# Performance work log

Hardware: AMD Instinct MI355X
Metric: run time of the kernel (lower is better)

## Reference

```python
import jax, jax.numpy as jnp
import numpy as np

N_HEADS = 16
N_KV_HEADS = 8
N_REP = 2
HEAD_DIM = 128
SOFTCAP = 50.0
NEG_INF = -2.3819763e38
ROPE_BASE = 10000.0


def _rotate_half(x):
    x1, x2 = jnp.split(x, 2, axis=-1)
    return jnp.concatenate((-x2, x1), axis=-1)


def _rope_cos_sin(seq_len, dtype):
    # Gemma2RotaryEmbedding: inv_freq over even dims, emb = cat(freqs, freqs)
    inv_freq = 1.0 / (ROPE_BASE ** (jnp.arange(0, HEAD_DIM, 2, dtype=jnp.float32) / HEAD_DIM))
    freqs = jnp.arange(seq_len, dtype=jnp.float32)[:, None] * inv_freq[None, :]  # [s, hd/2]
    emb = jnp.concatenate((freqs, freqs), axis=-1)  # [s, hd]
    return jnp.cos(emb).astype(dtype), jnp.sin(emb).astype(dtype)


def setup_inputs() -> dict:
    key = jax.random.key(0)
    ks = jax.random.split(key, 5)
    b, s, d = 2, 2048, 2048
    w_scale = 0.02
    return {
        "x": jax.random.normal(ks[0], (b, s, d), dtype=jnp.float32),
        "wq": jax.random.normal(ks[1], (N_HEADS * HEAD_DIM, d), dtype=jnp.float32) * w_scale,
        "wk": jax.random.normal(ks[2], (N_KV_HEADS * HEAD_DIM, d), dtype=jnp.float32) * w_scale,
        "wv": jax.random.normal(ks[3], (N_KV_HEADS * HEAD_DIM, d), dtype=jnp.float32) * w_scale,
        "wo": jax.random.normal(ks[4], (d, N_HEADS * HEAD_DIM), dtype=jnp.float32) * w_scale,
    }


def reference(x, wq, wk, wv, wo):
    b, s, d = x.shape
    # QKV projections (linear_fn = plain x @ W.T)
    xq = (x @ wq.T).reshape(b, s, N_HEADS, HEAD_DIM).transpose(0, 2, 1, 3)      # [b,h,s,hd]
    xk = (x @ wk.T).reshape(b, s, N_KV_HEADS, HEAD_DIM).transpose(0, 2, 1, 3)   # [b,kv,s,hd]
    xv = (x @ wv.T).reshape(b, s, N_KV_HEADS, HEAD_DIM).transpose(0, 2, 1, 3)
    # Gemma2 rotary on q, k
    cos, sin = _rope_cos_sin(s, x.dtype)  # [s,hd] each, broadcast over b,h
    xq = xq * cos + _rotate_half(xq) * sin
    xk = xk * cos + _rotate_half(xk) * sin
    # repeat_kv: expand kv heads to n_heads
    keys = jnp.repeat(xk, N_REP, axis=1)
    values = jnp.repeat(xv, N_REP, axis=1)
    # scores with scaling and Gemma2 logit softcapping
    scale = float(HEAD_DIM) ** -0.5
    scores = jnp.einsum("bhsd,bhtd->bhst", xq * scale, keys)
    scores = jnp.tanh(scores / SOFTCAP) * SOFTCAP
    # causal additive mask [s, t]
    q_pos = jnp.arange(s)[:, None]
    k_pos = jnp.arange(s)[None, :]
    mask = jnp.where(k_pos <= q_pos, 0.0, NEG_INF).astype(jnp.float32)
    scores = scores + mask  # broadcast over [b,h]
    probs = jax.nn.softmax(scores.astype(jnp.float32), axis=-1).astype(xq.dtype)
    out = jnp.einsum("bhst,bhtd->bhsd", probs, values)
    out = out.transpose(0, 2, 1, 3).reshape(b, s, N_HEADS * HEAD_DIM)
    return out @ wo.T
```

## Files before the change

kernel.cpp:

```cpp
#include <hip/hip_runtime.h>
#include <stdint.h>
#include <stddef.h>

#define S_LEN   2048
#define DMODEL  2048
#define NHEADS  16
#define NKVH    8
#define HD      128
#define QPRE 1.7677669529663688e-3f
#define C1 72.13475204444817f

typedef __attribute__((ext_vector_type(8))) short  short8;
typedef __attribute__((ext_vector_type(4))) float  float4v;

static __device__ __forceinline__ unsigned short f2bf(float f) {
  union { float f; unsigned int u; } v; v.f = f;
  unsigned int u = v.u;
  u += 0x7fffu + ((u >> 16) & 1u);
  return (unsigned short)(u >> 16);
}
static __device__ __forceinline__ float bf2f(unsigned short b) {
  union { unsigned int u; float f; } v; v.u = ((unsigned int)b) << 16;
  return v.f;
}
static __device__ __forceinline__ void gload_lds16(const void* g, void* l) {
  __builtin_amdgcn_global_load_lds(
      (const __attribute__((address_space(1))) void*)g,
      (__attribute__((address_space(3))) void*)l, 16, 0, 0);
}

__global__ __launch_bounds__(256) void cvt_all(
    const float* __restrict__ x,  const float* __restrict__ wq,
    const float* __restrict__ wk, const float* __restrict__ wv,
    const float* __restrict__ wo,
    ushort4* __restrict__ xb, ushort4* __restrict__ wcat,
    ushort4* __restrict__ wob) {
  int i = blockIdx.x * 256 + threadIdx.x;
  const float4* src; ushort4* dst; int j;
  if (i < 2097152)      { src = (const float4*)x;  dst = xb;             j = i; }
  else if (i < 3145728) { src = (const float4*)wq; dst = wcat;           j = i - 2097152; }
  else if (i < 3670016) { src = (const float4*)wk; dst = wcat + 1048576; j = i - 3145728; }
  else if (i < 4194304) { src = (const float4*)wv; dst = wcat + 1572864; j = i - 3670016; }
  else                  { src = (const float4*)wo; dst = wob;            j = i - 4194304; }
  float4 v = src[j];
  ushort4 o;
  o.x = f2bf(v.x); o.y = f2bf(v.y); o.z = f2bf(v.z); o.w = f2bf(v.w);
  dst[j] = o;
}

__global__ __launch_bounds__(256, 2) void gemm_bf16(
    const unsigned short* __restrict__ A,
    const unsigned short* __restrict__ B,
    void* __restrict__ Cout, int N, int mode) {
  const int t    = threadIdx.x;
  const int lane = t & 63;
  const int w    = t >> 6;
  const int l15  = lane & 15;
  const int quad = lane >> 4;
  const int m0   = blockIdx.y * 128;
  const int n0   = blockIdx.x * 128;
  const int wm   = (w >> 1) * 64;
  const int wn   = (w & 1) * 64;

  __shared__ unsigned short At[128 * 32];
  __shared__ unsigned short Bt[128 * 32];

  float4v acc[4][4];
#pragma unroll
  for (int mt = 0; mt < 4; ++mt)
#pragma unroll
    for (int nt = 0; nt < 4; ++nt)
      acc[mt][nt] = (float4v){0.f, 0.f, 0.f, 0.f};

  const unsigned short* Abase = A + (size_t)m0 * DMODEL;
  const unsigned short* Bbase = B + (size_t)n0 * DMODEL;
  const int srow = w * 16 + (lane >> 2);
  const int sch  = (lane & 3) * 8;

  for (int k0 = 0; k0 < DMODEL; k0 += 32) {
#pragma unroll
    for (int r = 0; r < 2; ++r) {
      gload_lds16(Abase + (size_t)(r * 64 + srow) * DMODEL + k0 + sch,
                  At + (r * 256 + w * 64) * 8);
      gload_lds16(Bbase + (size_t)(r * 64 + srow) * DMODEL + k0 + sch,
                  Bt + (r * 256 + w * 64) * 8);
    }
    __syncthreads();
    short8 af[4], bf[4];
#pragma unroll
    for (int mt = 0; mt < 4; ++mt)
      af[mt] = *(const short8*)(At + (wm + mt * 16 + l15) * 32 + quad * 8);
#pragma unroll
    for (int nt = 0; nt < 4; ++nt)
      bf[nt] = *(const short8*)(Bt + (wn + nt * 16 + l15) * 32 + quad * 8);
#pragma unroll
    for (int mt = 0; mt < 4; ++mt)
#pragma unroll
      for (int nt = 0; nt < 4; ++nt)
        acc[mt][nt] = __builtin_amdgcn_mfma_f32_16x16x32_bf16(
            af[mt], bf[nt], acc[mt][nt], 0, 0, 0);
    __syncthreads();
  }

  float* C = (float*)Cout;
#pragma unroll
  for (int mt = 0; mt < 4; ++mt) {
    int row = m0 + wm + mt * 16 + quad * 4;
#pragma unroll
    for (int nt = 0; nt < 4; ++nt) {
      int col = n0 + wn + nt * 16 + l15;
#pragma unroll
      for (int r2 = 0; r2 < 4; ++r2)
        C[(size_t)(row + r2) * N + col] = acc[mt][nt][r2];
    }
  }
}

__global__ __launch_bounds__(512, 2) void gemm256_qkv(
    const unsigned short* __restrict__ A,
    const unsigned short* __restrict__ B,
    unsigned short* __restrict__ C) {
  const int t    = threadIdx.x;
  const int lane = t & 63;
  const int w    = t >> 6;
  const int l15  = lane & 15;
  const int quad = lane >> 4;

  const int id  = blockIdx.x;
  const int swz = (id & 7) * 32 + (id >> 3);
  const int m0  = (swz >> 4) * 256;
  const int n0  = (swz & 15) * 256;

  __shared__ unsigned short sm[2][2][2][128 * 64];

  const int wm  = w >> 2;
  const int wnq = w & 3;
  const int hB  = wnq >> 1;
  const int wnl = (wnq & 1) * 64;

  int soff[2];
#pragma unroll
  for (int i = 0; i < 2; ++i) {
    int P = (w * 2 + i) * 64 + lane;
    int r = P >> 3;
    int lc = (P & 7) ^ (r & 7);
    soff[i] = r * DMODEL + lc * 8;
  }
  const unsigned short* Ab = A + (size_t)m0 * DMODEL;
  const unsigned short* Bb = B + (size_t)n0 * DMODEL;

  auto stage = [&](int mat, int half, int buf, int kt) {
    const unsigned short* g =
        (mat ? Bb : Ab) + (size_t)half * 128 * DMODEL + kt * 64;
    unsigned short* l = &sm[buf][mat][half][(w * 2) * 512];
#pragma unroll
    for (int i = 0; i < 2; ++i)
      gload_lds16(g + soff[i], l + i * 512);
  };

  float4v acc[2][2][4][2];
#pragma unroll
  for (int qm = 0; qm < 2; ++qm)
#pragma unroll
    for (int qn = 0; qn < 2; ++qn)
#pragma unroll
      for (int mt = 0; mt < 4; ++mt)
#pragma unroll
        for (int nt = 0; nt < 2; ++nt)
          acc[qm][qn][mt][nt] = (float4v){0.f, 0.f, 0.f, 0.f};

  stage(0, 0, 0, 0); stage(0, 1, 0, 0); stage(1, 0, 0, 0); stage(1, 1, 0, 0);
  stage(0, 0, 1, 1); stage(0, 1, 1, 1); stage(1, 0, 1, 1);
  asm volatile("s_waitcnt vmcnt(6)" ::: "memory");
  __builtin_amdgcn_s_barrier();

  const int NT = DMODEL / 64;
#pragma unroll 1
  for (int j = 0; j < NT; ++j) {
    const int c = j & 1;
    const unsigned short* As = &sm[c][0][wm][0];
    const unsigned short* Bs = &sm[c][1][hB][0];
    short8 af[4][2], ag[4][2], bf0[2][2], bf1[2][2];

    if (j + 1 < NT) stage(1, 1, c ^ 1, j + 1);

#pragma unroll
    for (int mt = 0; mt < 4; ++mt)
#pragma unroll
      for (int kk = 0; kk < 2; ++kk) {
        int r = mt * 16 + l15;
        af[mt][kk] = *(const short8*)&As[r * 64 + (((kk * 4 + quad) ^ (r & 7)) * 8)];
      }
#pragma unroll
    for (int nt = 0; nt < 2; ++nt)
#pragma unroll
      for (int kk = 0; kk < 2; ++kk) {
        int r = wnl + nt * 16 + l15;
        bf0[nt][kk] = *(const short8*)&Bs[r * 64 + (((kk * 4 + quad) ^ (r & 7)) * 8)];
      }
    __builtin_amdgcn_s_setprio(1);
#pragma unroll
    for (int mt = 0; mt < 4; ++mt)
#pragma unroll
      for (int nt = 0; nt < 2; ++nt)
#pragma unroll
        for (int kk = 0; kk < 2; ++kk)
          acc[0][0][mt][nt] = __builtin_amdgcn_mfma_f32_16x16x32_bf16(
              af[mt][kk], bf0[nt][kk], acc[0][0][mt][nt], 0, 0, 0);
    __builtin_amdgcn_s_setprio(0);

#pragma unroll
    for (int nt = 0; nt < 2; ++nt)
#pragma unroll
      for (int kk = 0; kk < 2; ++kk) {
        int r = wnl + 32 + nt * 16 + l15;
        bf1[nt][kk] = *(const short8*)&Bs[r * 64 + (((kk * 4 + quad) ^ (r & 7)) * 8)];
      }
    __builtin_amdgcn_s_setprio(1);
#pragma unroll
    for (int mt = 0; mt < 4; ++mt)
#pragma unroll
      for (int nt = 0; nt < 2; ++nt)
#pragma unroll
        for (int kk = 0; kk < 2; ++kk)
          acc[0][1][mt][nt] = __builtin_amdgcn_mfma_f32_16x16x32_bf16(
              af[mt][kk], bf1[nt][kk], acc[0][1][mt][nt], 0, 0, 0);
    __builtin_amdgcn_s_setprio(0);

#pragma unroll
    for (int mt = 0; mt < 4; ++mt)
#pragma unroll
      for (int kk = 0; kk < 2; ++kk) {
        int r = 64 + mt * 16 + l15;
        ag[mt][kk] = *(const short8*)&As[r * 64 + (((kk * 4 + quad) ^ (r & 7)) * 8)];
      }
    asm volatile("s_waitcnt lgkmcnt(0)" ::: "memory");
    __builtin_amdgcn_s_barrier();
    if (j + 2 < NT) {
      stage(0, 0, c, j + 2); stage(0, 1, c, j + 2); stage(1, 0, c, j + 2);
    }
    __builtin_amdgcn_s_setprio(1);
#pragma unroll
    for (int mt = 0; mt < 4; ++mt)
#pragma unroll
      for (int nt = 0; nt < 2; ++nt)
#pragma unroll
        for (int kk = 0; kk < 2; ++kk)
          acc[1][0][mt][nt] = __builtin_amdgcn_mfma_f32_16x16x32_bf16(
              ag[mt][kk], bf0[nt][kk], acc[1][0][mt][nt], 0, 0, 0);
#pragma unroll
    for (int mt = 0; mt < 4; ++mt)
#pragma unroll
      for (int nt = 0; nt < 2; ++nt)
#pragma unroll
        for (int kk = 0; kk < 2; ++kk)
          acc[1][1][mt][nt] = __builtin_amdgcn_mfma_f32_16x16x32_bf16(
              ag[mt][kk], bf1[nt][kk], acc[1][1][mt][nt], 0, 0, 0);
    __builtin_amdgcn_s_setprio(0);
    if (j + 2 < NT)      { asm volatile("s_waitcnt vmcnt(6)" ::: "memory"); }
    else if (j + 1 < NT) { asm volatile("s_waitcnt vmcnt(0)" ::: "memory"); }
    __builtin_amdgcn_s_barrier();
  }

#pragma unroll
  for (int qm = 0; qm < 2; ++qm)
#pragma unroll
    for (int mt = 0; mt < 4; ++mt) {
      int row0 = m0 + wm * 128 + qm * 64 + mt * 16 + quad * 4;
      int b = row0 >> 11, s0 = row0 & (S_LEN - 1);
#pragma unroll
      for (int qn = 0; qn < 2; ++qn)
#pragma unroll
        for (int nt = 0; nt < 2; ++nt) {
          int col = n0 + wnq * 64 + qn * 32 + nt * 16 + l15;
          float4v v = acc[qm][qn][mt][nt];
          if (col < 2048) {
            int head = col >> 7, d = col & (HD - 1);
#pragma unroll
            for (int r2 = 0; r2 < 4; ++r2)
              C[((size_t)(b * 16 + head) * S_LEN + s0 + r2) * HD + d] = f2bf(v[r2]);
          } else if (col < 3072) {
            int c2 = col - 2048;
            int kvh = c2 >> 7, d = c2 & (HD - 1);
#pragma unroll
            for (int r2 = 0; r2 < 4; ++r2)
              C[8388608 + ((size_t)(b * 8 + kvh) * S_LEN + s0 + r2) * HD + d] = f2bf(v[r2]);
          } else {
            int c2 = col - 3072;
            int kvh = c2 >> 7, d = c2 & (HD - 1);
            ushort4 pk;
            pk.x = f2bf(v[0]); pk.y = f2bf(v[1]);
            pk.z = f2bf(v[2]); pk.w = f2bf(v[3]);
            *(ushort4*)&C[12582912 + ((size_t)(b * 8 + kvh) * HD + d) * S_LEN + s0] = pk;
          }
        }
    }
}

__global__ __launch_bounds__(256) void rope_kernel(unsigned short* __restrict__ Q,
                                                   unsigned short* __restrict__ Kc) {
  int gt = blockIdx.x * 256 + threadIdx.x;
  int r = gt >> 6;
  int j = gt & 63;
  const int QROWS = 2 * NHEADS * S_LEN;
  bool isQ = (r < QROWS);
  unsigned short* p = isQ ? (Q + (size_t)r * HD)
                          : (Kc + (size_t)(r - QROWS) * HD);
  int pos = r & (S_LEN - 1);
  float inv = exp2f(-(float)j * 0.20762050593046868f);
  float ang = (float)pos * inv;
  float c = cosf(ang), s = sinf(ang);
  float sc = isQ ? QPRE : 1.0f;
  float x1 = bf2f(p[j]), x2 = bf2f(p[j + 64]);
  p[j]      = f2bf((x1 * c - x2 * s) * sc);
  p[j + 64] = f2bf((x2 * c + x1 * s) * sc);
}

__global__ __launch_bounds__(256, 2) void attn_kernel(
    const unsigned short* __restrict__ Q,
    const unsigned short* __restrict__ Kc,
    const unsigned short* __restrict__ Vt,
    unsigned short* __restrict__ Aout) {
  const int t    = threadIdx.x;
  const int lane = t & 63;
  const int w    = t >> 6;
  const int l15  = lane & 15;
  const int quad = lane >> 4;
  const int bh = blockIdx.x;
  const int pp = blockIdx.y;
  const int b = bh >> 4, h = bh & 15, kv = h >> 1;
  const int qtA = pp, qtB = 31 - pp;
  const int q0A = qtA * 64, q0B = qtB * 64;
  const int ntB = qtB + 1;

  __shared__ unsigned short Kt[64 * 128];
  __shared__ unsigned short Vts[128 * 64];
  __shared__ unsigned short Pt[4 * 2 * 1024];

  int offK[4], offV[4];
#pragma unroll
  for (int i = 0; i < 4; ++i) {
    int g = i * 256 + t;
    int rK = g >> 4, cK = (g & 15) ^ (rK & 7);
    offK[i] = rK * HD + cK * 8;
    int rV = g >> 3, cV = (g & 7) ^ (rV & 7);
    offV[i] = rV * S_LEN + cV * 8;
  }

  const unsigned short* QA = Q + ((size_t)(b * NHEADS + h) * S_LEN + q0A + w * 16) * HD;
  const unsigned short* QB = Q + ((size_t)(b * NHEADS + h) * S_LEN + q0B + w * 16) * HD;
  short8 qfA[4], qfB[4];
#pragma unroll
  for (int kk = 0; kk < 4; ++kk) {
    qfA[kk] = *(const short8*)&QA[l15 * HD + kk * 32 + quad * 8];
    qfB[kk] = *(const short8*)&QB[l15 * HD + kk * 32 + quad * 8];
  }

  float4v oA[8], oB[8];
#pragma unroll
  for (int nth = 0; nth < 8; ++nth) {
    oA[nth] = (float4v){0.f, 0.f, 0.f, 0.f};
    oB[nth] = (float4v){0.f, 0.f, 0.f, 0.f};
  }
  float lsA = 0.f, lsB = 0.f;

  const unsigned short* kg0 = Kc + (size_t)(b * NKVH + kv) * S_LEN * HD;
  const unsigned short* vg0 = Vt + (size_t)(b * NKVH + kv) * HD * S_LEN;
  unsigned short* PB = Pt + (w * 2 + 0) * 1024;
  unsigned short* PA = Pt + (w * 2 + 1) * 1024;

  auto stage = [&](int kt) {
    const unsigned short* kgp = kg0 + (size_t)kt * 64 * HD;
    const unsigned short* vgp = vg0 + (size_t)kt * 64;
#pragma unroll
    for (int i = 0; i < 4; ++i)
      gload_lds16(kgp + offK[i], &Kt[(i * 256 + w * 64) * 8]);
#pragma unroll
    for (int i = 0; i < 4; ++i)
      gload_lds16(vgp + offV[i], &Vts[(i * 256 + w * 64) * 8]);
  };

  auto softcap = [&](float x) -> float {
    float xx = __builtin_amdgcn_fmed3f(x, -0.26f, 0.26f);
    float x2 = xx * xx;
    float u = __builtin_fmaf(0.13333334f, x2, -0.33333334f);
    float v = __builtin_fmaf(u, x2, 1.0f);
    return __builtin_amdgcn_exp2f((C1 * xx) * v);
  };

  stage(0);
  for (int kt = 0; kt < ntB; ++kt) {
    __syncthreads();
    const bool doA   = (kt <= qtA);
    const bool diagA = (kt == qtA);
    const bool diagB = (kt == qtB);
    const unsigned short* Kb = Kt;
    const unsigned short* Vb = Vts;

#pragma unroll
    for (int ntk = 0; ntk < 4; ++ntk) {
      int pb = l15 * 64 + (((ntk * 2 + (quad >> 1)) ^ (l15 & 7)) * 8) + (quad & 1) * 4;
      short8 kf[4];
#pragma unroll
      for (int kk = 0; kk < 4; ++kk)
        kf[kk] = *(const short8*)
            &Kb[(ntk * 16 + l15) * HD + (((kk * 4 + quad) ^ (l15 & 7)) * 8)];

      if (diagB && (ntk * 16 > w * 16 + 15)) {
        uint2 z; z.x = 0u; z.y = 0u;
        *(uint2*)&PB[pb] = z;
      } else {
        float4v s0 = (float4v){0.f, 0.f, 0.f, 0.f};
#pragma unroll
        for (int kk = 0; kk < 4; ++kk)
          s0 = __builtin_amdgcn_mfma_f32_16x16x32_bf16(kf[kk], qfB[kk], s0, 0, 0, 0);
        float pv[4];
#pragma unroll
        for (int r = 0; r < 4; ++r) {
          float p = softcap(s0[r]);
          if (diagB)
            p = (ntk * 16 + quad * 4 + r <= w * 16 + l15) ? p : 0.f;
          lsB += p;
          pv[r] = p;
        }
        union { float f; unsigned u; } u0, u1, u2, u3;
        u0.f = pv[0]; u1.f = pv[1]; u2.f = pv[2]; u3.f = pv[3];
        uint2 pk;
        pk.x = __builtin_amdgcn_perm(u1.u, u0.u, 0x07060302);
        pk.y = __builtin_amdgcn_perm(u3.u, u2.u, 0x07060302);
        *(uint2*)&PB[pb] = pk;
      }

      if (doA) {
        if (diagA && (ntk * 16 > w * 16 + 15)) {
          uint2 z; z.x = 0u; z.y = 0u;
          *(uint2*)&PA[pb] = z;
        } else {
          float4v s0 = (float4v){0.f, 0.f, 0.f, 0.f};
#pragma unroll
          for (int kk = 0; kk < 4; ++kk)
            s0 = __builtin_amdgcn_mfma_f32_16x16x32_bf16(kf[kk], qfA[kk], s0, 0, 0, 0);
          float pv[4];
#pragma unroll
          for (int r = 0; r < 4; ++r) {
            float p = softcap(s0[r]);
            if (diagA)
              p = (ntk * 16 + quad * 4 + r <= w * 16 + l15) ? p : 0.f;
            lsA += p;
            pv[r] = p;
          }
          union { float f; unsigned u; } u0, u1, u2, u3;
          u0.f = pv[0]; u1.f = pv[1]; u2.f = pv[2]; u3.f = pv[3];
          uint2 pk;
          pk.x = __builtin_amdgcn_perm(u1.u, u0.u, 0x07060302);
          pk.y = __builtin_amdgcn_perm(u3.u, u2.u, 0x07060302);
          *(uint2*)&PA[pb] = pk;
        }
      }
    }

#pragma unroll
    for (int kk = 0; kk < 2; ++kk) {
      int sw = ((kk * 4 + quad) ^ (l15 & 7)) * 8;
      short8 pB0 = *(const short8*)&PB[l15 * 64 + sw];
      short8 pA0;
      if (doA) pA0 = *(const short8*)&PA[l15 * 64 + sw];
#pragma unroll
      for (int nth = 0; nth < 8; ++nth) {
        short8 vf = *(const short8*)&Vb[(nth * 16 + l15) * 64 + sw];
        oB[nth] = __builtin_amdgcn_mfma_f32_16x16x32_bf16(pB0, vf, oB[nth], 0, 0, 0);
        if (doA)
          oA[nth] = __builtin_amdgcn_mfma_f32_16x16x32_bf16(pA0, vf, oA[nth], 0, 0, 0);
      }
    }
    __syncthreads();
    if (kt + 1 < ntB) stage(kt + 1);
  }

#pragma unroll
  for (int tile = 0; tile < 2; ++tile) {
    float ls = tile ? lsA : lsB;
    float4v* oo = tile ? oA : oB;
    int q0 = tile ? q0A : q0B;
    float v = ls;
    v += __shfl_xor(v, 16, 64);
    v += __shfl_xor(v, 32, 64);
    float inv = __builtin_amdgcn_rcpf(v);
    float iv[4];
#pragma unroll
    for (int r = 0; r < 4; ++r) iv[r] = __shfl(inv, quad * 4 + r, 64);
    unsigned short* ob = Aout + (size_t)(b * S_LEN + q0 + w * 16) * DMODEL + h * HD;
#pragma unroll
    for (int nth = 0; nth < 8; ++nth) {
#pragma unroll
      for (int r = 0; r < 4; ++r) {
        int row = quad * 4 + r;
        ob[(size_t)row * DMODEL + nth * 16 + l15] = f2bf(oo[nth][r] * iv[r]);
      }
    }
  }
}

extern "C" void kernel_launch(void* const* d_in, const int* in_sizes, int n_in,
                              void* d_out, int out_size, void* d_ws, size_t ws_size,
                              hipStream_t stream) {
  const float* x  = (const float*)d_in[0];
  const float* wq = (const float*)d_in[1];
  const float* wk = (const float*)d_in[2];
  const float* wv = (const float*)d_in[3];
  const float* wo = (const float*)d_in[4];

  char* ws = (char*)d_ws;
  unsigned short* xb   = (unsigned short*)(ws + 0);
  unsigned short* wcat = (unsigned short*)(ws + 16777216);
  unsigned short* wob  = (unsigned short*)(ws + 33554432);
  unsigned short* QKV  = (unsigned short*)(ws + 41943040);
  unsigned short* AO   = (unsigned short*)(ws + 75497472);

  unsigned short* Qw = QKV;
  unsigned short* Kw = QKV + 8388608;
  unsigned short* Vw = QKV + 12582912;

  cvt_all<<<20480, 256, 0, stream>>>(x, wq, wk, wv, wo,
                                     (ushort4*)xb, (ushort4*)wcat, (ushort4*)wob);

  gemm256_qkv<<<256, 512, 0, stream>>>(xb, wcat, QKV);

  rope_kernel<<<24576, 256, 0, stream>>>(Qw, Kw);

  attn_kernel<<<dim3(32, 16), 256, 0, stream>>>(Qw, Kw, Vw, AO);

  gemm_bf16<<<dim3(16, 32), 256, 0, stream>>>(AO, wob, d_out, 2048, 2);
}
```

Baseline: 312.7 us.

## Restructure attention to one q-tile per block with two waves of 32 rows

Replaces the paired causal q-tile scheme (tiles p and 31-p per 256-thread block) with one 64-row q-tile per 128-thread block. Each wave now handles 32 query rows and reuses each K fragment across two MFMA streams, and the grid doubles to 32x32. This reduces per-block register pressure and drops the branchy A/B logic. In exchange it gives up the pairing that balanced causal work across blocks, so block lengths become uneven, and each block now stages the full K/V tile with only two waves.

After: 324.1 us. 3.6% more time.

```diff
diff --git a/kernel.cpp b/kernel.cpp
--- a/kernel.cpp
+++ b/kernel.cpp
@@ -316,7 +316,7 @@
   p[j + 64] = f2bf((x2 * c + x1 * s) * sc);
 }
 
-__global__ __launch_bounds__(256, 2) void attn_kernel(
+__global__ __launch_bounds__(128, 2) void attn_kernel(
     const unsigned short* __restrict__ Q,
     const unsigned short* __restrict__ Kc,
     const unsigned short* __restrict__ Vt,
@@ -327,57 +327,54 @@
   const int l15  = lane & 15;
   const int quad = lane >> 4;
   const int bh = blockIdx.x;
-  const int pp = blockIdx.y;
+  const int qt = blockIdx.y;
   const int b = bh >> 4, h = bh & 15, kv = h >> 1;
-  const int qtA = pp, qtB = 31 - pp;
-  const int q0A = qtA * 64, q0B = qtB * 64;
-  const int ntB = qtB + 1;
+  const int q0 = qt * 64;
+  const int ntK = qt + 1;
 
   __shared__ unsigned short Kt[64 * 128];
   __shared__ unsigned short Vts[128 * 64];
-  __shared__ unsigned short Pt[4 * 2 * 1024];
-
-  int offK[4], offV[4];
-#pragma unroll
-  for (int i = 0; i < 4; ++i) {
-    int g = i * 256 + t;
+  __shared__ unsigned short Pt[2 * 2048];
+
+  int offK[8], offV[8];
+#pragma unroll
+  for (int i = 0; i < 8; ++i) {
+    int g = i * 128 + t;
     int rK = g >> 4, cK = (g & 15) ^ (rK & 7);
     offK[i] = rK * HD + cK * 8;
     int rV = g >> 3, cV = (g & 7) ^ (rV & 7);
     offV[i] = rV * S_LEN + cV * 8;
   }
 
-  const unsigned short* QA = Q + ((size_t)(b * NHEADS + h) * S_LEN + q0A + w * 16) * HD;
-  const unsigned short* QB = Q + ((size_t)(b * NHEADS + h) * S_LEN + q0B + w * 16) * HD;
-  short8 qfA[4], qfB[4];
-#pragma unroll
-  for (int kk = 0; kk < 4; ++kk) {
-    qfA[kk] = *(const short8*)&QA[l15 * HD + kk * 32 + quad * 8];
-    qfB[kk] = *(const short8*)&QB[l15 * HD + kk * 32 + quad * 8];
-  }
-
-  float4v oA[8], oB[8];
-#pragma unroll
-  for (int nth = 0; nth < 8; ++nth) {
-    oA[nth] = (float4v){0.f, 0.f, 0.f, 0.f};
-    oB[nth] = (float4v){0.f, 0.f, 0.f, 0.f};
-  }
-  float lsA = 0.f, lsB = 0.f;
+  const unsigned short* QB = Q + ((size_t)(b * NHEADS + h) * S_LEN + q0 + w * 32) * HD;
+  short8 qf[2][4];
+#pragma unroll
+  for (int ntq = 0; ntq < 2; ++ntq)
+#pragma unroll
+    for (int kk = 0; kk < 4; ++kk)
+      qf[ntq][kk] = *(const short8*)&QB[(ntq * 16 + l15) * HD + kk * 32 + quad * 8];
+
+  float4v oo[2][8];
+#pragma unroll
+  for (int ntq = 0; ntq < 2; ++ntq)
+#pragma unroll
+    for (int nth = 0; nth < 8; ++nth)
+      oo[ntq][nth] = (float4v){0.f, 0.f, 0.f, 0.f};
+  float ls[2] = {0.f, 0.f};
 
   const unsigned short* kg0 = Kc + (size_t)(b * NKVH + kv) * S_LEN * HD;
   const unsigned short* vg0 = Vt + (size_t)(b * NKVH + kv) * HD * S_LEN;
-  unsigned short* PB = Pt + (w * 2 + 0) * 1024;
-  unsigned short* PA = Pt + (w * 2 + 1) * 1024;
+  unsigned short* PB = Pt + w * 2048;
 
   auto stage = [&](int kt) {
     const unsigned short* kgp = kg0 + (size_t)kt * 64 * HD;
     const unsigned short* vgp = vg0 + (size_t)kt * 64;
 #pragma unroll
-    for (int i = 0; i < 4; ++i)
-      gload_lds16(kgp + offK[i], &Kt[(i * 256 + w * 64) * 8]);
-#pragma unroll
-    for (int i = 0; i < 4; ++i)
-      gload_lds16(vgp + offV[i], &Vts[(i * 256 + w * 64) * 8]);
+    for (int i = 0; i < 8; ++i)
+      gload_lds16(kgp + offK[i], &Kt[(i * 128 + w * 64) * 8]);
+#pragma unroll
+    for (int i = 0; i < 8; ++i)
+      gload_lds16(vgp + offV[i], &Vts[(i * 128 + w * 64) * 8]);
   };
 
   auto softcap = [&](float x) -> float {
@@ -389,64 +386,38 @@
   };
 
   stage(0);
-  for (int kt = 0; kt < ntB; ++kt) {
+  for (int kt = 0; kt < ntK; ++kt) {
     __syncthreads();
-    const bool doA   = (kt <= qtA);
-    const bool diagA = (kt == qtA);
-    const bool diagB = (kt == qtB);
-    const unsigned short* Kb = Kt;
-    const unsigned short* Vb = Vts;
+    const bool diag = (kt == qt);
 
 #pragma unroll
     for (int ntk = 0; ntk < 4; ++ntk) {
       int pb = l15 * 64 + (((ntk * 2 + (quad >> 1)) ^ (l15 & 7)) * 8) + (quad & 1) * 4;
-      short8 kf[4];
-#pragma unroll
-      for (int kk = 0; kk < 4; ++kk)
-        kf[kk] = *(const short8*)
-            &Kb[(ntk * 16 + l15) * HD + (((kk * 4 + quad) ^ (l15 & 7)) * 8)];
-
-      if (diagB && (ntk * 16 > w * 16 + 15)) {
+      if (diag && (ntk * 16 > w * 32 + 31)) {
         uint2 z; z.x = 0u; z.y = 0u;
-        *(uint2*)&PB[pb] = z;
+        *(uint2*)&PB[pb] = z; *(uint2*)&PB[pb + 1024] = z;
       } else {
-        float4v s0 = (float4v){0.f, 0.f, 0.f, 0.f};
+        short8 kf[4];
 #pragma unroll
         for (int kk = 0; kk < 4; ++kk)
-          s0 = __builtin_amdgcn_mfma_f32_16x16x32_bf16(kf[kk], qfB[kk], s0, 0, 0, 0);
-        float pv[4];
-#pragma unroll
-        for (int r = 0; r < 4; ++r) {
-          float p = softcap(s0[r]);
-          if (diagB)
-            p = (ntk * 16 + quad * 4 + r <= w * 16 + l15) ? p : 0.f;
-          lsB += p;
-          pv[r] = p;
+          kf[kk] = *(const short8*)
+              &Kt[(ntk * 16 + l15) * HD + (((kk * 4 + quad) ^ (l15 & 7)) * 8)];
+        float4v s0 = (float4v){0.f, 0.f, 0.f, 0.f}, s1 = s0;
+#pragma unroll
+        for (int kk = 0; kk < 4; ++kk) {
+          s0 = __builtin_amdgcn_mfma_f32_16x16x32_bf16(kf[kk], qf[0][kk], s0, 0, 0, 0);
+          s1 = __builtin_amdgcn_mfma_f32_16x16x32_bf16(kf[kk], qf[1][kk], s1, 0, 0, 0);
         }
-        union { float f; unsigned u; } u0, u1, u2, u3;
-        u0.f = pv[0]; u1.f = pv[1]; u2.f = pv[2]; u3.f = pv[3];
-        uint2 pk;
-        pk.x = __builtin_amdgcn_perm(u1.u, u0.u, 0x07060302);
-        pk.y = __builtin_amdgcn_perm(u3.u, u2.u, 0x07060302);
-        *(uint2*)&PB[pb] = pk;
-      }
-
-      if (doA) {
-        if (diagA && (ntk * 16 > w * 16 + 15)) {
-          uint2 z; z.x = 0u; z.y = 0u;
-          *(uint2*)&PA[pb] = z;
-        } else {
-          float4v s0 = (float4v){0.f, 0.f, 0.f, 0.f};
-#pragma unroll
-          for (int kk = 0; kk < 4; ++kk)
-            s0 = __builtin_amdgcn_mfma_f32_16x16x32_bf16(kf[kk], qfA[kk], s0, 0, 0, 0);
+#pragma unroll
+        for (int ntq = 0; ntq < 2; ++ntq) {
+          const float4v& sv = ntq ? s1 : s0;
           float pv[4];
 #pragma unroll
           for (int r = 0; r < 4; ++r) {
-            float p = softcap(s0[r]);
-            if (diagA)
-              p = (ntk * 16 + quad * 4 + r <= w * 16 + l15) ? p : 0.f;
-            lsA += p;
+            float p = softcap(sv[r]);
+            if (diag)
+              p = (ntk * 16 + quad * 4 + r <= w * 32 + ntq * 16 + l15) ? p : 0.f;
+            ls[ntq] += p;
             pv[r] = p;
           }
           union { float f; unsigned u; } u0, u1, u2, u3;
@@ -454,7 +425,7 @@
           uint2 pk;
           pk.x = __builtin_amdgcn_perm(u1.u, u0.u, 0x07060302);
           pk.y = __builtin_amdgcn_perm(u3.u, u2.u, 0x07060302);
-          *(uint2*)&PA[pb] = pk;
+          *(uint2*)&PB[pb + ntq * 1024] = pk;
         }
       }
     }
@@ -462,40 +433,39 @@
 #pragma unroll
     for (int kk = 0; kk < 2; ++kk) {
       int sw = ((kk * 4 + quad) ^ (l15 & 7)) * 8;
-      short8 pB0 = *(const short8*)&PB[l15 * 64 + sw];
-      short8 pA0;
-      if (doA) pA0 = *(const short8*)&PA[l15 * 64 + sw];
+      short8 p0 = *(const short8*)&PB[l15 * 64 + sw];
+      short8 p1 = *(const short8*)&PB[(16 + l15) * 64 + sw];
 #pragma unroll
       for (int nth = 0; nth < 8; ++nth) {
-        short8 vf = *(const short8*)&Vb[(nth * 16 + l15) * 64 + sw];
-        oB[nth] = __builtin_amdgcn_mfma_f32_16x16x32_bf16(pB0, vf, oB[nth], 0, 0, 0);
-        if (doA)
-          oA[nth] = __builtin_amdgcn_mfma_f32_16x16x32_bf16(pA0, vf, oA[nth], 0, 0, 0);
+        short8 vf = *(const short8*)&Vts[(nth * 16 + l15) * 64 + sw];
+        oo[0][nth] = __builtin_amdgcn_mfma_f32_16x16x32_bf16(p0, vf, oo[0][nth], 0, 0, 0);
+        oo[1][nth] = __builtin_amdgcn_mfma_f32_16x16x32_bf16(p1, vf, oo[1][nth], 0, 0, 0);
       }
     }
     __syncthreads();
-    if (kt + 1 < ntB) stage(kt + 1);
-  }
-
-#pragma unroll
-  for (int tile = 0; tile < 2; ++tile) {
-    float ls = tile ? lsA : lsB;
-    float4v* oo = tile ? oA : oB;
-    int q0 = tile ? q0A : q0B;
-    float v = ls;
+    if (kt + 1 < ntK) stage(kt + 1);
+  }
+
+  float inv[2];
+#pragma unroll
+  for (int ntq = 0; ntq < 2; ++ntq) {
+    float v = ls[ntq];
     v += __shfl_xor(v, 16, 64);
     v += __shfl_xor(v, 32, 64);
-    float inv = __builtin_amdgcn_rcpf(v);
+    inv[ntq] = __builtin_amdgcn_rcpf(v);
+  }
+  unsigned short* ob = Aout + (size_t)(b * S_LEN + q0 + w * 32) * DMODEL + h * HD;
+#pragma unroll
+  for (int ntq = 0; ntq < 2; ++ntq) {
     float iv[4];
 #pragma unroll
-    for (int r = 0; r < 4; ++r) iv[r] = __shfl(inv, quad * 4 + r, 64);
-    unsigned short* ob = Aout + (size_t)(b * S_LEN + q0 + w * 16) * DMODEL + h * HD;
+    for (int r = 0; r < 4; ++r) iv[r] = __shfl(inv[ntq], quad * 4 + r, 64);
 #pragma unroll
     for (int nth = 0; nth < 8; ++nth) {
 #pragma unroll
       for (int r = 0; r < 4; ++r) {
-        int row = quad * 4 + r;
-        ob[(size_t)row * DMODEL + nth * 16 + l15] = f2bf(oo[nth][r] * iv[r]);
+        int row = ntq * 16 + quad * 4 + r;
+        ob[(size_t)row * DMODEL + nth * 16 + l15] = f2bf(oo[ntq][nth][r] * iv[r]);
       }
     }
   }
@@ -528,7 +498,7 @@
 
   rope_kernel<<<24576, 256, 0, stream>>>(Qw, Kw);
 
-  attn_kernel<<<dim3(32, 16), 256, 0, stream>>>(Qw, Kw, Vw, AO);
+  attn_kernel<<<dim3(32, 32), 128, 0, stream>>>(Qw, Kw, Vw, AO);
 
   gemm_bf16<<<dim3(16, 32), 256, 0, stream>>>(AO, wob, d_out, 2048, 2);
 }
```

## Replace output projection GEMM with double-buffered 256x128 swizzled MFMA kernel

Applied to the files above, without the earlier changes.

The simple 128x128 output-projection GEMM, which reloaded LDS with K=32 steps and two full barriers per step, is replaced by a 512-thread 256x128 tile kernel. The new kernel uses K=64 steps, XOR-swizzled LDS layout to avoid bank conflicts, and double-buffered async global-to-LDS loads that overlap with MFMA work. It also adds a block-id swizzle for L2 locality and raises wave priority around the MFMA section. This brings higher register and LDS use per block and relies on hand-placed waitcnt counts being correct.

Measured after the change: 306.7 us. Within noise of the previous version (-1.9%).

```diff
diff --git a/kernel.cpp b/kernel.cpp
--- a/kernel.cpp
+++ b/kernel.cpp
@@ -48,74 +48,6 @@
   dst[j] = o;
 }
 
-__global__ __launch_bounds__(256, 2) void gemm_bf16(
-    const unsigned short* __restrict__ A,
-    const unsigned short* __restrict__ B,
-    void* __restrict__ Cout, int N, int mode) {
-  const int t    = threadIdx.x;
-  const int lane = t & 63;
-  const int w    = t >> 6;
-  const int l15  = lane & 15;
-  const int quad = lane >> 4;
-  const int m0   = blockIdx.y * 128;
-  const int n0   = blockIdx.x * 128;
-  const int wm   = (w >> 1) * 64;
-  const int wn   = (w & 1) * 64;
-
-  __shared__ unsigned short At[128 * 32];
-  __shared__ unsigned short Bt[128 * 32];
-
-  float4v acc[4][4];
-#pragma unroll
-  for (int mt = 0; mt < 4; ++mt)
-#pragma unroll
-    for (int nt = 0; nt < 4; ++nt)
-      acc[mt][nt] = (float4v){0.f, 0.f, 0.f, 0.f};
-
-  const unsigned short* Abase = A + (size_t)m0 * DMODEL;
-  const unsigned short* Bbase = B + (size_t)n0 * DMODEL;
-  const int srow = w * 16 + (lane >> 2);
-  const int sch  = (lane & 3) * 8;
-
-  for (int k0 = 0; k0 < DMODEL; k0 += 32) {
-#pragma unroll
-    for (int r = 0; r < 2; ++r) {
-      gload_lds16(Abase + (size_t)(r * 64 + srow) * DMODEL + k0 + sch,
-                  At + (r * 256 + w * 64) * 8);
-      gload_lds16(Bbase + (size_t)(r * 64 + srow) * DMODEL + k0 + sch,
-                  Bt + (r * 256 + w * 64) * 8);
-    }
-    __syncthreads();
-    short8 af[4], bf[4];
-#pragma unroll
-    for (int mt = 0; mt < 4; ++mt)
-      af[mt] = *(const short8*)(At + (wm + mt * 16 + l15) * 32 + quad * 8);
-#pragma unroll
-    for (int nt = 0; nt < 4; ++nt)
-      bf[nt] = *(const short8*)(Bt + (wn + nt * 16 + l15) * 32 + quad * 8);
-#pragma unroll
-    for (int mt = 0; mt < 4; ++mt)
-#pragma unroll
-      for (int nt = 0; nt < 4; ++nt)
-        acc[mt][nt] = __builtin_amdgcn_mfma_f32_16x16x32_bf16(
-            af[mt], bf[nt], acc[mt][nt], 0, 0, 0);
-    __syncthreads();
-  }
-
-  float* C = (float*)Cout;
-#pragma unroll
-  for (int mt = 0; mt < 4; ++mt) {
-    int row = m0 + wm + mt * 16 + quad * 4;
-#pragma unroll
-    for (int nt = 0; nt < 4; ++nt) {
-      int col = n0 + wn + nt * 16 + l15;
-#pragma unroll
-      for (int r2 = 0; r2 < 4; ++r2)
-        C[(size_t)(row + r2) * N + col] = acc[mt][nt][r2];
-    }
-  }
-}
-
 __global__ __launch_bounds__(512, 2) void gemm256_qkv(
     const unsigned short* __restrict__ A,
     const unsigned short* __restrict__ B,
@@ -295,6 +227,115 @@
           }
         }
     }
+}
+
+__global__ __launch_bounds__(512, 2) void gemm256_out(
+    const unsigned short* __restrict__ A,
+    const unsigned short* __restrict__ B,
+    float* __restrict__ C) {
+  const int t    = threadIdx.x;
+  const int lane = t & 63;
+  const int w    = t >> 6;
+  const int l15  = lane & 15;
+  const int quad = lane >> 4;
+
+  const int id  = blockIdx.x;
+  const int swz = (id & 7) * 32 + (id >> 3);
+  const int m0  = (swz >> 4) * 256;
+  const int n0  = (swz & 15) * 128;
+
+  __shared__ unsigned short sm[2][3][128 * 64];
+
+  const int wm = w >> 1;
+  const int wn = w & 1;
+  const int hA = wm >> 1;
+  const int ra0 = (wm & 1) * 64;
+
+  int soff[2];
+#pragma unroll
+  for (int i = 0; i < 2; ++i) {
+    int P = (w * 2 + i) * 64 + lane;
+    int r = P >> 3;
+    int lc = (P & 7) ^ (r & 7);
+    soff[i] = r * DMODEL + lc * 8;
+  }
+  const unsigned short* Ab = A + (size_t)m0 * DMODEL;
+  const unsigned short* Bb = B + (size_t)n0 * DMODEL;
+
+  auto stage = [&](int region, int buf, int kt) {
+    const unsigned short* g =
+        (region == 2 ? Bb : Ab + (size_t)region * 128 * DMODEL) + kt * 64;
+    unsigned short* l = &sm[buf][region][(w * 2) * 512];
+#pragma unroll
+    for (int i = 0; i < 2; ++i)
+      gload_lds16(g + soff[i], l + i * 512);
+  };
+
+  float4v acc[4][4];
+#pragma unroll
+  for (int mt = 0; mt < 4; ++mt)
+#pragma unroll
+    for (int nt = 0; nt < 4; ++nt)
+      acc[mt][nt] = (float4v){0.f, 0.f, 0.f, 0.f};
+
+  stage(0, 0, 0); stage(1, 0, 0); stage(2, 0, 0);
+  stage(0, 1, 1); stage(1, 1, 1); stage(2, 1, 1);
+  asm volatile("s_waitcnt vmcnt(6)" ::: "memory");
+  __builtin_amdgcn_s_barrier();
+
+  const int NT = DMODEL / 64;
+#pragma unroll 1
+  for (int j = 0; j < NT; ++j) {
+    const int c = j & 1;
+    const unsigned short* As = &sm[c][hA][0];
+    const unsigned short* Bs = &sm[c][2][0];
+    short8 af[4][2], bf[4][2];
+
+#pragma unroll
+    for (int mt = 0; mt < 4; ++mt)
+#pragma unroll
+      for (int kk = 0; kk < 2; ++kk) {
+        int r = ra0 + mt * 16 + l15;
+        af[mt][kk] = *(const short8*)&As[r * 64 + (((kk * 4 + quad) ^ (r & 7)) * 8)];
+      }
+#pragma unroll
+    for (int nt = 0; nt < 4; ++nt)
+#pragma unroll
+      for (int kk = 0; kk < 2; ++kk) {
+        int r = wn * 64 + nt * 16 + l15;
+        bf[nt][kk] = *(const short8*)&Bs[r * 64 + (((kk * 4 + quad) ^ (r & 7)) * 8)];
+      }
+    asm volatile("s_waitcnt lgkmcnt(0)" ::: "memory");
+    __builtin_amdgcn_s_barrier();
+    if (j + 2 < NT) { stage(0, c, j + 2); stage(1, c, j + 2); stage(2, c, j + 2); }
+
+    __builtin_amdgcn_s_setprio(1);
+#pragma unroll
+    for (int mt = 0; mt < 4; ++mt)
+#pragma unroll
+      for (int nt = 0; nt < 4; ++nt)
+#pragma unroll
+        for (int kk = 0; kk < 2; ++kk)
+          acc[mt][nt] = __builtin_amdgcn_mfma_f32_16x16x32_bf16(
+              af[mt][kk], bf[nt][kk], acc[mt][nt], 0, 0, 0);
+    __builtin_amdgcn_s_setprio(0);
+
+    if (j + 2 < NT)      { asm volatile("s_waitcnt vmcnt(6)" ::: "memory"); }
+    else if (j + 1 < NT) { asm volatile("s_waitcnt vmcnt(0)" ::: "memory"); }
+    __builtin_amdgcn_s_barrier();
+  }
+
+#pragma unroll
+  for (int mt = 0; mt < 4; ++mt) {
+    int row = m0 + wm * 64 + mt * 16 + quad * 4;
+#pragma unroll
+    for (int nt = 0; nt < 4; ++nt) {
+      int col = n0 + wn * 64 + nt * 16 + l15;
+#pragma unroll
+      for (int r2 = 0; r2 < 4; ++r2)
+        C[(size_t)(row + r2) * 2048 + col] = acc[mt][nt][r2];
+    }
+  }
 }
 
 __global__ __launch_bounds__(256) void rope_kernel(unsigned short* __restrict__ Q,
@@ -530,5 +571,5 @@
 
   attn_kernel<<<dim3(32, 16), 256, 0, stream>>>(Qw, Kw, Vw, AO);
 
-  gemm_bf16<<<dim3(16, 32), 256, 0, stream>>>(AO, wob, d_out, 2048, 2);
-}
+  gemm256_out<<<256, 512, 0, stream>>>(AO, wob, (float*)d_out);
+}
```
